# Performance work log

Measured on AMD Instinct MI355X. Metric: run time of the kernel, lower is better.

The kernel has to match this reference:

```python
import jax, jax.numpy as jnp
import numpy as np

N, L, H, M, D = 4096, 4096, 8, 64, 64

def setup_inputs() -> dict:
    key = jax.random.key(0)
    kq, kk, kv = jax.random.split(key, 3)
    queries = jax.random.normal(kq, (N, H, M), dtype=jnp.float32)
    keys = jax.random.normal(kk, (L, H, M), dtype=jnp.float32)
    values = jax.random.normal(kv, (L, H, D), dtype=jnp.float32)
    return {"queries": queries, "keys": keys, "values": values}

def reference(queries, keys, values):
    # scores: [n, l, h] = sigmoid(q . k) per head
    attention_num = jax.nn.sigmoid(jnp.einsum('nhm,lhm->nlh', queries, keys))
    # normalizer: sum over l -> [n, h] (torch code broadcasts via wasteful repeat)
    attention_normalizer = jnp.sum(attention_num, axis=1, keepdims=True)  # [n,1,h]
    attention = attention_num / attention_normalizer  # [n,l,h]
    # dropout p=0.0 -> identity
    attn_output = jnp.einsum('nlh,lhd->nhd', attention, values)
    return attn_output
```

## Files before the change

### kernel.cpp

```cpp
#include <hip/hip_runtime.h>
#include <stdint.h>


typedef __bf16 bf16x8 __attribute__((ext_vector_type(8)));
typedef __bf16 bf16x2 __attribute__((ext_vector_type(2)));
typedef float  f32x2  __attribute__((ext_vector_type(2)));
typedef float  f32x16 __attribute__((ext_vector_type(16)));

constexpr int NH = 8, MD = 64, NL = 4096, NN = 4096;
constexpr size_t ONUM_ELEMS = (size_t)NN * NH * MD;
constexpr size_t Z_ELEMS    = (size_t)NN * NH;
constexpr size_t KB_ELEMS   = (size_t)NH * NL * MD;
constexpr size_t VTB_ELEMS  = (size_t)NH * NL * MD;

__device__ __forceinline__ unsigned packbf2(float a, float b) {
  bf16x2 t = __builtin_convertvector((f32x2){a, b}, bf16x2);
  return __builtin_bit_cast(unsigned, t);
}

__device__ __forceinline__ void glds16(const void* g, void* l) {
  __builtin_amdgcn_global_load_lds(
      (const __attribute__((address_space(1))) unsigned int*)g,
      (__attribute__((address_space(3))) unsigned int*)l, 16, 0, 0);
}

__global__ __launch_bounds__(256) void diffattn_prepass(
    const float* __restrict__ Kg, const float* __restrict__ Vg,
    unsigned short* __restrict__ Kb, unsigned short* __restrict__ Vtb) {
  __shared__ __attribute__((aligned(16))) unsigned short Vt_lds[64 * 64];
  const int tid = threadIdx.x;
  const int h = blockIdx.x & 7;
  const int t = blockIdx.x >> 3;

#pragma unroll
  for (int e = 0; e < 2; ++e) {
    const int g = tid * 2 + e;
    const int l = g >> 3, c = g & 7;
    const float* kp = Kg + (((size_t)(t * 64 + l) * NH + h) * MD) + c * 8;
    const float4 a = *(const float4*)kp;
    const float4 b = *(const float4*)(kp + 4);
    unsigned out[4] = {packbf2(a.x, a.y), packbf2(a.z, a.w),
                       packbf2(b.x, b.y), packbf2(b.z, b.w)};
    unsigned short* dst =
        Kb + ((size_t)h * NL + t * 64 + l) * MD + ((c ^ (l & 7)) * 8);
    *(uint4*)dst = *(const uint4*)out;
  }

  {
    const int lr = tid & 63, dbase = (tid >> 6) * 16;
    const float* vp = Vg + (((size_t)(t * 64 + lr) * NH + h) * MD) + dbase;
#pragma unroll
    for (int i = 0; i < 4; ++i) {
      const float4 v = *(const float4*)(vp + i * 4);
      const int d0 = dbase + i * 4;
      Vt_lds[(d0 + 0) * 64 + lr] = __builtin_bit_cast(unsigned short, (__bf16)v.x);
      Vt_lds[(d0 + 1) * 64 + lr] = __builtin_bit_cast(unsigned short, (__bf16)v.y);
      Vt_lds[(d0 + 2) * 64 + lr] = __builtin_bit_cast(unsigned short, (__bf16)v.z);
      Vt_lds[(d0 + 3) * 64 + lr] = __builtin_bit_cast(unsigned short, (__bf16)v.w);
    }
  }
  __syncthreads();
#pragma unroll
  for (int e = 0; e < 2; ++e) {
    const int g = tid * 2 + e;
    const int d = g >> 3, cl = g & 7;
    const uint4 chunk = *(const uint4*)&Vt_lds[d * 64 + cl * 8];
    unsigned short* dst = Vtb + ((size_t)(h * 64 + t) * 64 + d) * 64 +
                          ((cl ^ (d & 7)) * 8);
    *(uint4*)dst = chunk;
  }
}

__global__ __launch_bounds__(256, 4) void diffattn_partial(
    const float* __restrict__ Qg, const unsigned short* __restrict__ Kb,
    const unsigned short* __restrict__ Vtb, float* __restrict__ Onum,
    float* __restrict__ Zp, int nsplit, int lLen) {
  __shared__ __attribute__((aligned(16))) unsigned short Ksh[2][64 * 64];
  __shared__ __attribute__((aligned(16))) unsigned short Vtsh[2][64 * 64];

  const int tid  = threadIdx.x;
  const int w    = tid >> 6;
  const int lane = tid & 63;
  const int col  = lane & 31;
  const int hi   = lane >> 5;

  const int h     = blockIdx.x & 7;
  const int tmp   = blockIdx.x >> 3;
  const int split = tmp % nsplit;
  const int n0    = (tmp / nsplit) * 128;
  const int lBeg  = split * lLen;

  bf16x8 qf[4];
  {
    const float* qp = Qg + ((size_t)(n0 + w * 32 + col) * NH + h) * MD;
    const float c = -1.4426950408889634f;
#pragma unroll
    for (int kc = 0; kc < 4; ++kc) {
      const float4 x = *(const float4*)(qp + kc * 16 + hi * 8);
      const float4 y = *(const float4*)(qp + kc * 16 + hi * 8 + 4);
      bf16x8 f;
      f[0] = (__bf16)(c * x.x); f[1] = (__bf16)(c * x.y);
      f[2] = (__bf16)(c * x.z); f[3] = (__bf16)(c * x.w);
      f[4] = (__bf16)(c * y.x); f[5] = (__bf16)(c * y.y);
      f[6] = (__bf16)(c * y.z); f[7] = (__bf16)(c * y.w);
      qf[kc] = f;
    }
  }

  f32x16 oacc[2];
#pragma unroll
  for (int i = 0; i < 16; ++i) { oacc[0][i] = 0.f; oacc[1][i] = 0.f; }
  float zacc = 0.f;
  const f32x16 zf = {};

  const char* kgh = (const char*)(Kb + (size_t)h * NL * MD);
  const char* vgh = (const char*)(Vtb + (size_t)h * NL * MD);
  const int o = w * 2048 + lane * 16;
  const int T = lLen >> 6;

  {
    const char* kgb = kgh + (size_t)lBeg * 128;
    const char* vgb = vgh + (size_t)lBeg * 128;
    glds16(kgb + o,        (char*)Ksh[0]  + w * 2048);
    glds16(kgb + o + 1024, (char*)Ksh[0]  + w * 2048 + 1024);
    glds16(vgb + o,        (char*)Vtsh[0] + w * 2048);
    glds16(vgb + o + 1024, (char*)Vtsh[0] + w * 2048 + 1024);
  }

  for (int t = 0; t < T; ++t) {
    const int cur = t & 1;
    __syncthreads();
    if (t + 1 < T) {
      const char* kgb = kgh + (size_t)(lBeg + (t + 1) * 64) * 128;
      const char* vgb = vgh + (size_t)(lBeg + (t + 1) * 64) * 128;
      glds16(kgb + o,        (char*)Ksh[cur ^ 1]  + w * 2048);
      glds16(kgb + o + 1024, (char*)Ksh[cur ^ 1]  + w * 2048 + 1024);
      glds16(vgb + o,        (char*)Vtsh[cur ^ 1] + w * 2048);
      glds16(vgb + o + 1024, (char*)Vtsh[cur ^ 1] + w * 2048 + 1024);
    }

    f32x16 d1[2];
#pragma unroll
    for (int lh = 0; lh < 2; ++lh) {
      const int rowK = lh * 32 + col;
      const char* kp = (const char*)Ksh[cur] + rowK * 128;
      const int sw = rowK & 7;
      {
        const bf16x8 kf = *(const bf16x8*)(kp + ((hi ^ sw) * 16));
        d1[lh] = __builtin_amdgcn_mfma_f32_32x32x16_bf16(kf, qf[0], zf, 0, 0, 0);
      }
#pragma unroll
      for (int kc = 1; kc < 4; ++kc) {
        const bf16x8 kf = *(const bf16x8*)(kp + (((kc << 1) | hi) ^ sw) * 16);
        d1[lh] = __builtin_amdgcn_mfma_f32_32x32x16_bf16(kf, qf[kc], d1[lh], 0, 0, 0);
      }
    }

    unsigned pk[2][8];
#pragma unroll
    for (int lh = 0; lh < 2; ++lh) {
      float s[16];
#pragma unroll
      for (int r = 0; r < 16; ++r) {
        const float e = __builtin_amdgcn_exp2f(d1[lh][r]);
        s[r] = __builtin_amdgcn_rcpf(1.0f + e);
        zacc += s[r];
      }
#pragma unroll
      for (int p = 0; p < 8; ++p) pk[lh][p] = packbf2(s[2 * p], s[2 * p + 1]);
    }

#pragma unroll
    for (int kc2 = 0; kc2 < 4; ++kc2) {
      const int lh = kc2 >> 1, s4 = (kc2 & 1) * 4;
      const unsigned send0 = hi ? pk[lh][s4 + 0] : pk[lh][s4 + 2];
      const unsigned send1 = hi ? pk[lh][s4 + 1] : pk[lh][s4 + 3];
      const unsigned recv0 = (unsigned)__shfl_xor((int)send0, 32, 64);
      const unsigned recv1 = (unsigned)__shfl_xor((int)send1, 32, 64);
      union { unsigned u[4]; bf16x8 v; } pf;
      if (hi == 0) {
        pf.u[0] = pk[lh][s4 + 0]; pf.u[1] = pk[lh][s4 + 1];
        pf.u[2] = recv0;          pf.u[3] = recv1;
      } else {
        pf.u[0] = recv0;          pf.u[1] = recv1;
        pf.u[2] = pk[lh][s4 + 2]; pf.u[3] = pk[lh][s4 + 3];
      }
#pragma unroll
      for (int ds = 0; ds < 2; ++ds) {
        const int rowV = ds * 32 + col;
        const bf16x8 vf =
            *(const bf16x8*)((const char*)Vtsh[cur] + rowV * 128 +
                             (((kc2 << 1) | hi) ^ (rowV & 7)) * 16);
        oacc[ds] = __builtin_amdgcn_mfma_f32_32x32x16_bf16(pf.v, vf, oacc[ds], 0, 0, 0);
      }
    }
  }

  const float zrow = zacc + __shfl_xor(zacc, 32, 64);
  if (hi == 0)
    Zp[(size_t)split * Z_ELEMS + (size_t)(n0 + w * 32 + col) * NH + h] = zrow;

  float* onum = Onum + (size_t)split * ONUM_ELEMS;
#pragma unroll
  for (int ds = 0; ds < 2; ++ds) {
    const int d = ds * 32 + col;
#pragma unroll
    for (int r = 0; r < 16; ++r) {
      const int row = (r & 3) + 8 * (r >> 2) + 4 * hi;
      onum[((size_t)(n0 + w * 32 + row) * NH + h) * MD + d] = oacc[ds][r];
    }
  }
}

__global__ __launch_bounds__(256) void diffattn_combine(
    const float* __restrict__ Onum, const float* __restrict__ Zp,
    float* __restrict__ Og, int nsplit) {
  const int idx = blockIdx.x * 256 + threadIdx.x;
  if (idx >= (int)(ONUM_ELEMS / 4)) return;
  const int nh = idx >> 4;
  const int d4 = (idx & 15) * 4;
  float z = 0.f;
  float4 o = make_float4(0.f, 0.f, 0.f, 0.f);
  for (int s = 0; s < nsplit; ++s) {
    z += Zp[(size_t)s * Z_ELEMS + nh];
    const float4 t = *(const float4*)(Onum + (size_t)s * ONUM_ELEMS +
                                      (size_t)nh * MD + d4);
    o.x += t.x; o.y += t.y; o.z += t.z; o.w += t.w;
  }
  const float zi = __builtin_amdgcn_rcpf(z);
  float4 r = make_float4(o.x * zi, o.y * zi, o.z * zi, o.w * zi);
  *(float4*)(Og + (size_t)nh * MD + d4) = r;
}

extern "C" void kernel_launch(void* const* d_in, const int* in_sizes, int n_in,
                              void* d_out, int out_size, void* d_ws, size_t ws_size,
                              hipStream_t stream) {
  const float* Q = (const float*)d_in[0];
  const float* K = (const float*)d_in[1];
  const float* V = (const float*)d_in[2];
  float* O = (float*)d_out;

  const size_t conv_bytes = (KB_ELEMS + VTB_ELEMS) * sizeof(unsigned short);
  int nsplit = 4;
  while (nsplit > 1 &&
         (size_t)nsplit * (ONUM_ELEMS + Z_ELEMS) * sizeof(float) + conv_bytes >
             ws_size)
    nsplit >>= 1;

  float* Onum = (float*)d_ws;
  float* Zp   = Onum + (size_t)nsplit * ONUM_ELEMS;
  unsigned short* Kbb = (unsigned short*)(Zp + (size_t)nsplit * Z_ELEMS);
  unsigned short* Vtb = Kbb + KB_ELEMS;

  const int lLen = NL / nsplit;
  diffattn_prepass<<<dim3(8 * (NL / 64)), dim3(256), 0, stream>>>(K, V, Kbb, Vtb);
  diffattn_partial<<<dim3(8 * 32 * nsplit), dim3(256), 0, stream>>>(
      Q, Kbb, Vtb, Onum, Zp, nsplit, lLen);
  diffattn_combine<<<dim3((ONUM_ELEMS / 4 + 255) / 256), dim3(256), 0, stream>>>(
      Onum, Zp, O, nsplit);
}
```

Before: 132.0 us.

## Permute V transpose layout to drop cross-lane shuffles in PV MFMA

The preprocessing kernel now stores V^T rows with a bit-permuted L index, so the P fragment each lane already holds from the QK MFMA output lines up directly with the V operand. This removes the per-step __shfl_xor exchanges and selects used to build the P operand. V fragments are also loaded earlier, before the sigmoid computation, to hide LDS latency. The trade-off is a few more live registers for the prefetched V fragments.

```diff
diff --git a/kernel.cpp b/kernel.cpp
--- a/kernel.cpp
+++ b/kernel.cpp
@@ -6,6 +6,7 @@
 typedef __bf16 bf16x2 __attribute__((ext_vector_type(2)));
 typedef float  f32x2  __attribute__((ext_vector_type(2)));
 typedef float  f32x16 __attribute__((ext_vector_type(16)));
+typedef unsigned u32x4 __attribute__((ext_vector_type(4)));
 
 constexpr int NH = 8, MD = 64, NL = 4096, NN = 4096;
 constexpr size_t ONUM_ELEMS = (size_t)NN * NH * MD;
@@ -48,15 +49,16 @@
 
   {
     const int lr = tid & 63, dbase = (tid >> 6) * 16;
+    const int pl = (lr & 0x33) | ((lr & 4) << 1) | ((lr & 8) >> 1);
     const float* vp = Vg + (((size_t)(t * 64 + lr) * NH + h) * MD) + dbase;
 #pragma unroll
     for (int i = 0; i < 4; ++i) {
       const float4 v = *(const float4*)(vp + i * 4);
       const int d0 = dbase + i * 4;
-      Vt_lds[(d0 + 0) * 64 + lr] = __builtin_bit_cast(unsigned short, (__bf16)v.x);
-      Vt_lds[(d0 + 1) * 64 + lr] = __builtin_bit_cast(unsigned short, (__bf16)v.y);
-      Vt_lds[(d0 + 2) * 64 + lr] = __builtin_bit_cast(unsigned short, (__bf16)v.z);
-      Vt_lds[(d0 + 3) * 64 + lr] = __builtin_bit_cast(unsigned short, (__bf16)v.w);
+      Vt_lds[(d0 + 0) * 64 + pl] = __builtin_bit_cast(unsigned short, (__bf16)v.x);
+      Vt_lds[(d0 + 1) * 64 + pl] = __builtin_bit_cast(unsigned short, (__bf16)v.y);
+      Vt_lds[(d0 + 2) * 64 + pl] = __builtin_bit_cast(unsigned short, (__bf16)v.z);
+      Vt_lds[(d0 + 3) * 64 + pl] = __builtin_bit_cast(unsigned short, (__bf16)v.w);
     }
   }
   __syncthreads();
@@ -117,6 +119,7 @@
   const char* vgh = (const char*)(Vtb + (size_t)h * NL * MD);
   const int o = w * 2048 + lane * 16;
   const int T = lLen >> 6;
+  const int sw = col & 7;
 
   {
     const char* kgb = kgh + (size_t)lBeg * 128;
@@ -144,17 +147,28 @@
     for (int lh = 0; lh < 2; ++lh) {
       const int rowK = lh * 32 + col;
       const char* kp = (const char*)Ksh[cur] + rowK * 128;
-      const int sw = rowK & 7;
+      const int swk = rowK & 7;
       {
-        const bf16x8 kf = *(const bf16x8*)(kp + ((hi ^ sw) * 16));
+        const bf16x8 kf = *(const bf16x8*)(kp + ((hi ^ swk) * 16));
         d1[lh] = __builtin_amdgcn_mfma_f32_32x32x16_bf16(kf, qf[0], zf, 0, 0, 0);
       }
 #pragma unroll
       for (int kc = 1; kc < 4; ++kc) {
-        const bf16x8 kf = *(const bf16x8*)(kp + (((kc << 1) | hi) ^ sw) * 16);
+        const bf16x8 kf = *(const bf16x8*)(kp + (((kc << 1) | hi) ^ swk) * 16);
         d1[lh] = __builtin_amdgcn_mfma_f32_32x32x16_bf16(kf, qf[kc], d1[lh], 0, 0, 0);
       }
     }
+
+    const char* vb = (const char*)Vtsh[cur];
+    bf16x8 vfA[2][2];
+#pragma unroll
+    for (int c = 0; c < 2; ++c)
+#pragma unroll
+      for (int ds = 0; ds < 2; ++ds) {
+        const int rowV = ds * 32 + col;
+        vfA[c][ds] = *(const bf16x8*)(vb + rowV * 128 +
+                                      (((c << 1) | hi) ^ (rowV & 7)) * 16);
+      }
 
     unsigned pk[2][8];
 #pragma unroll
@@ -171,28 +185,30 @@
     }
 
 #pragma unroll
-    for (int kc2 = 0; kc2 < 4; ++kc2) {
-      const int lh = kc2 >> 1, s4 = (kc2 & 1) * 4;
-      const unsigned send0 = hi ? pk[lh][s4 + 0] : pk[lh][s4 + 2];
-      const unsigned send1 = hi ? pk[lh][s4 + 1] : pk[lh][s4 + 3];
-      const unsigned recv0 = (unsigned)__shfl_xor((int)send0, 32, 64);
-      const unsigned recv1 = (unsigned)__shfl_xor((int)send1, 32, 64);
-      union { unsigned u[4]; bf16x8 v; } pf;
-      if (hi == 0) {
-        pf.u[0] = pk[lh][s4 + 0]; pf.u[1] = pk[lh][s4 + 1];
-        pf.u[2] = recv0;          pf.u[3] = recv1;
-      } else {
-        pf.u[0] = recv0;          pf.u[1] = recv1;
-        pf.u[2] = pk[lh][s4 + 2]; pf.u[3] = pk[lh][s4 + 3];
-      }
+    for (int c = 0; c < 2; ++c) {
+      const bf16x8 pf =
+          __builtin_bit_cast(bf16x8, *(const u32x4*)&pk[0][c * 4]);
+#pragma unroll
+      for (int ds = 0; ds < 2; ++ds)
+        oacc[ds] = __builtin_amdgcn_mfma_f32_32x32x16_bf16(pf, vfA[c][ds],
+                                                           oacc[ds], 0, 0, 0);
+    }
+#pragma unroll
+    for (int c = 0; c < 2; ++c)
 #pragma unroll
       for (int ds = 0; ds < 2; ++ds) {
         const int rowV = ds * 32 + col;
-        const bf16x8 vf =
-            *(const bf16x8*)((const char*)Vtsh[cur] + rowV * 128 +
-                             (((kc2 << 1) | hi) ^ (rowV & 7)) * 16);
-        oacc[ds] = __builtin_amdgcn_mfma_f32_32x32x16_bf16(pf.v, vf, oacc[ds], 0, 0, 0);
-      }
+        vfA[c][ds] = *(const bf16x8*)(vb + rowV * 128 +
+                                      ((((c + 2) << 1 | hi)) ^ (rowV & 7)) * 16);
+      }
+#pragma unroll
+    for (int c = 0; c < 2; ++c) {
+      const bf16x8 pf =
+          __builtin_bit_cast(bf16x8, *(const u32x4*)&pk[1][c * 4]);
+#pragma unroll
+      for (int ds = 0; ds < 2; ++ds)
+        oacc[ds] = __builtin_amdgcn_mfma_f32_32x32x16_bf16(pf, vfA[c][ds],
+                                                           oacc[ds], 0, 0, 0);
     }
   }
 
```

After: 126.0 us. 4.5% less time.
